# Kernel optimization log

Hardware: AMD Instinct MI355X
Metric: run time of the kernel (lower is better)

Reference implementation:

```python
import jax, jax.numpy as jnp
import numpy as np

B, S, D = 2, 2048, 512
H = 8
HD = D // H  # head dim = 64


def setup_inputs() -> dict:
    key = jax.random.key(0)
    ks = jax.random.split(key, 4)
    scale = 1.0 / np.sqrt(D)
    x = jax.random.normal(ks[0], (B, S, D), dtype=jnp.float32)
    wq = jax.random.normal(ks[1], (D, D), dtype=jnp.float32) * scale
    wk = jax.random.normal(ks[2], (D, D), dtype=jnp.float32) * scale
    wv = jax.random.normal(ks[3], (D, D), dtype=jnp.float32) * scale
    bq = jnp.zeros((D,), dtype=jnp.float32)
    bk = jnp.zeros((D,), dtype=jnp.float32)
    bv = jnp.zeros((D,), dtype=jnp.float32)
    return {"x": x, "wq": wq, "bq": bq, "wk": wk, "bk": bk, "wv": wv, "bv": bv}


def reference(x, wq, bq, wk, bk, wv, bv):
    # Linear projections (torch Linear: y = x @ W^T + b; weights here stored as [out,in])
    q = x @ wq.T + bq  # [B,S,D]
    k = x @ wk.T + bk
    v = x @ wv.T + bv
    # split heads -> [B,H,S,HD]
    q = q.reshape(B, S, H, HD).transpose(0, 2, 1, 3)
    k = k.reshape(B, S, H, HD).transpose(0, 2, 1, 3)
    v = v.reshape(B, S, H, HD).transpose(0, 2, 1, 3)
    # QK^T scores, scaled by 1/sqrt(head_dim)
    scores = jnp.einsum("bhqd,bhkd->bhqk", q, k) / jnp.sqrt(jnp.float32(HD))
    # softmax-free: elementwise sigmoid instead of softmax normalization
    attn = jax.nn.sigmoid(scores)  # [B,H,S,S] — the memory-bound intermediate
    out = jnp.einsum("bhqk,bhkd->bhqd", attn, v)
    # merge heads -> [B,S,D]
    return out.transpose(0, 2, 1, 3).reshape(B, S, D)
```

## Files before the change

kernel.cpp:

```cpp
#include <hip/hip_runtime.h>
#include <cstdint>
#include <cstddef>

#define BB   2
#define SS   2048
#define DD   512
#define HH   8
#define HDIM 64
#define XN   ((size_t)BB * SS * DD)
#define WN   ((size_t)DD * DD)

typedef __attribute__((ext_vector_type(8)))  short          s16x8;
typedef __attribute__((ext_vector_type(8)))  unsigned short u16x8;
typedef __attribute__((ext_vector_type(16))) float          f32x16;

static __device__ __forceinline__ unsigned short f2bf(float f) {
  union { float f; unsigned u; } x; x.f = f;
  unsigned r = x.u + 0x7fffu + ((x.u >> 16) & 1u);
  return (unsigned short)(r >> 16);
}
static __device__ __forceinline__ unsigned packtrunc(float lo, float hi) {
  return __builtin_amdgcn_perm(__float_as_uint(hi), __float_as_uint(lo), 0x07060302u);
}

#define QSCALE (-0.18033688011111543f)

__global__ __launch_bounds__(256) void cvt_kernel(
    const float* __restrict__ x,
    const float* __restrict__ wq, const float* __restrict__ wk, const float* __restrict__ wv,
    unsigned short* __restrict__ xb, unsigned short* __restrict__ wb3) {
  const int y = blockIdx.y;
  const float* src; unsigned short* dst;
  if (y == 0) { src = x; dst = xb; }
  else {
    if (blockIdx.x >= 256) return;
    src = (y == 1) ? wq : (y == 2) ? wk : wv;
    dst = wb3 + (size_t)(y - 1) * WN;
  }
  int i = (blockIdx.x * 256 + threadIdx.x) * 4;
  float4 f = *(const float4*)(src + i);
  ushort4 o;
  o.x = f2bf(f.x); o.y = f2bf(f.y); o.z = f2bf(f.z); o.w = f2bf(f.w);
  *(ushort4*)(dst + i) = o;
}

__global__ __launch_bounds__(256) void proj_kernel(
    const unsigned short* __restrict__ xb, const unsigned short* __restrict__ wb3,
    const float* __restrict__ bq, const float* __restrict__ bk, const float* __restrict__ bv,
    unsigned short* __restrict__ qo, unsigned short* __restrict__ ko,
    unsigned short* __restrict__ vt) {
  __shared__ unsigned short As[2][128 * 40];
  __shared__ unsigned short Bs[2][64 * 40];

  const int z = blockIdx.z;
  const unsigned short* w = wb3 + (size_t)z * WN;
  const float* bias = (z == 0) ? bq : (z == 1) ? bk : bv;

  const int t = threadIdx.x;
  const int lane = t & 63, wave = t >> 6;
  const int ln = lane & 31, hi = lane >> 5;
  const int m0 = blockIdx.x * 128, n0 = blockIdx.y * 64;

  u16x8 ar[2], br;
#pragma unroll
  for (int i = 0; i < 2; i++) {
    int c = t + i * 256;
    ar[i] = *(const u16x8*)&xb[(size_t)(m0 + (c >> 2)) * DD + (c & 3) * 8];
  }
  br = *(const u16x8*)&w[(size_t)(n0 + (t >> 2)) * DD + (t & 3) * 8];
#pragma unroll
  for (int i = 0; i < 2; i++) {
    int c = t + i * 256;
    *(u16x8*)&As[0][(c >> 2) * 40 + (c & 3) * 8] = ar[i];
  }
  *(u16x8*)&Bs[0][(t >> 2) * 40 + (t & 3) * 8] = br;
  __syncthreads();

  f32x16 acc0 = {}, acc1 = {};

#pragma unroll 2
  for (int kt = 0; kt < 16; kt++) {
    const int cur = kt & 1, nxt = cur ^ 1;
    if (kt < 15) {
      int k0 = (kt + 1) * 32;
#pragma unroll
      for (int i = 0; i < 2; i++) {
        int c = t + i * 256;
        ar[i] = *(const u16x8*)&xb[(size_t)(m0 + (c >> 2)) * DD + k0 + (c & 3) * 8];
      }
      br = *(const u16x8*)&w[(size_t)(n0 + (t >> 2)) * DD + k0 + (t & 3) * 8];
    }
#pragma unroll
    for (int cc = 0; cc < 2; cc++) {
      s16x8 af = *(const s16x8*)&As[cur][(wave * 32 + ln) * 40 + cc * 16 + hi * 8];
      s16x8 b0 = *(const s16x8*)&Bs[cur][(ln) * 40 + cc * 16 + hi * 8];
      s16x8 b1 = *(const s16x8*)&Bs[cur][(32 + ln) * 40 + cc * 16 + hi * 8];
      acc0 = __builtin_amdgcn_mfma_f32_32x32x16_bf16(af, b0, acc0, 0, 0, 0);
      acc1 = __builtin_amdgcn_mfma_f32_32x32x16_bf16(af, b1, acc1, 0, 0, 0);
    }
    if (kt < 15) {
#pragma unroll
      for (int i = 0; i < 2; i++) {
        int c = t + i * 256;
        *(u16x8*)&As[nxt][(c >> 2) * 40 + (c & 3) * 8] = ar[i];
      }
      *(u16x8*)&Bs[nxt][(t >> 2) * 40 + (t & 3) * 8] = br;
    }
    __syncthreads();
  }

  const int h = blockIdx.y;
  const int bidx = m0 >> 11;
  const int sbase = (m0 & 2047) + wave * 32;
  const size_t bhb = (size_t)(bidx * HH + h) * SS * HDIM;
  const int kts = sbase >> 5;

#pragma unroll
  for (int nh = 0; nh < 2; nh++) {
    f32x16 acc = nh ? acc1 : acc0;
    const int hd = nh * 32 + ln;
    const float bval = bias[n0 + hd];

    if (z == 0) {
#pragma unroll
      for (int r = 0; r < 16; r++) {
        int s = sbase + (r & 3) + 8 * (r >> 2) + 4 * hi;
        qo[bhb + (size_t)s * HDIM + hd] = f2bf((acc[r] + bval) * QSCALE);
      }
    } else if (z == 1) {
      const int c = hd >> 4, hk = (hd >> 3) & 1, j = hd & 7;
      unsigned short* kd = ko + bhb + ((size_t)kts * 4 + c) * 512 + j;
#pragma unroll
      for (int r = 0; r < 16; r++) {
        int off = (r & 3) + 8 * (r >> 2) + 4 * hi;
        kd[(hk * 32 + off) * 8] = f2bf(acc[r] + bval);
      }
    } else {
      unsigned short* vd = vt + bhb + ((size_t)kts * 4 + nh * 2) * 512 + hi * 256 + ln * 8;
#pragma unroll
      for (int g = 0; g < 4; g++) {
        unsigned short* vg = vd + (g >> 1) * 512 + (g & 1) * 4;
#pragma unroll
        for (int j = 0; j < 4; j += 2) {
          unsigned pk = (unsigned)f2bf(acc[g * 4 + j] + bval) |
                        ((unsigned)f2bf(acc[g * 4 + j + 1] + bval) << 16);
          *(unsigned*)&vg[j] = pk;
        }
      }
    }
  }
}

__global__ __launch_bounds__(512, 4) void attn_kernel(
    const unsigned short* __restrict__ qb,
    const unsigned short* __restrict__ kfb,
    const unsigned short* __restrict__ vfb,
    float* __restrict__ out) {
  __shared__ __align__(16) float red[2 * 4096];

  const int t = threadIdx.x;
  const int lane = t & 63, wave = t >> 6;
  const int ln = lane & 31, hi = lane >> 5;
  const int qh = wave & 1, kh = wave >> 1;
  const int fid = blockIdx.y * 32 + blockIdx.x;
  const int bh = fid & 15, qx = fid >> 4;
  const int b = bh >> 3, h = bh & 7;
  const unsigned short* qp = qb + (size_t)bh * SS * HDIM;
  const unsigned short* kfp = kfb + (size_t)bh * SS * HDIM;
  const unsigned short* vfp = vfb + (size_t)bh * SS * HDIM;
  const int q0 = qx * 64;

  s16x8 qf[4];
#pragma unroll
  for (int c = 0; c < 4; c++)
    qf[c] = *(const s16x8*)&qp[(size_t)(q0 + qh * 32 + ln) * HDIM + c * 16 + hi * 8];

  f32x16 o0 = {}, o1 = {};

  s16x8 kf[4], vf[4];
  int foff = kh * 16 * 2048 + lane * 8;
#pragma unroll
  for (int c = 0; c < 4; c++) {
    kf[c] = *(const s16x8*)&kfp[foff + c * 512];
    vf[c] = *(const s16x8*)&vfp[foff + c * 512];
  }
  foff += 2048;

#pragma unroll 1
  for (int i = 0; i < 16; i++) {
    f32x16 st = {};
#pragma unroll
    for (int c = 0; c < 4; c++)
      st = __builtin_amdgcn_mfma_f32_32x32x16_bf16(kf[c], qf[c], st, 0, 0, 0);

    if (i < 15) {
#pragma unroll
      for (int c = 0; c < 4; c++)
        kf[c] = *(const s16x8*)&kfp[foff + c * 512];
    }

    unsigned pg[8];
#pragma unroll
    for (int g = 0; g < 4; g++) {
      float p0 = __builtin_amdgcn_rcpf(1.0f + __builtin_amdgcn_exp2f(st[4 * g + 0]));
      float p1 = __builtin_amdgcn_rcpf(1.0f + __builtin_amdgcn_exp2f(st[4 * g + 1]));
      float p2 = __builtin_amdgcn_rcpf(1.0f + __builtin_amdgcn_exp2f(st[4 * g + 2]));
      float p3 = __builtin_amdgcn_rcpf(1.0f + __builtin_amdgcn_exp2f(st[4 * g + 3]));
      pg[2 * g]     = packtrunc(p0, p1);
      pg[2 * g + 1] = packtrunc(p2, p3);
    }

#pragma unroll
    for (int c = 0; c < 2; c++) {
      union { unsigned u[4]; s16x8 v; } pu;
      pu.u[0] = pg[4 * c + 0];
      pu.u[1] = pg[4 * c + 1];
      pu.u[2] = pg[4 * c + 2];
      pu.u[3] = pg[4 * c + 3];
      o0 = __builtin_amdgcn_mfma_f32_32x32x16_bf16(pu.v, vf[c], o0, 0, 0, 0);
      o1 = __builtin_amdgcn_mfma_f32_32x32x16_bf16(pu.v, vf[2 + c], o1, 0, 0, 0);
    }

    if (i < 15) {
#pragma unroll
      for (int c = 0; c < 4; c++)
        vf[c] = *(const s16x8*)&vfp[foff + c * 512];
      foff += 2048;
    }
  }

  if (kh >= 2) {
    const int slot = kh - 2;
#pragma unroll
    for (int dh = 0; dh < 2; dh++) {
      f32x16 ov = dh ? o1 : o0;
#pragma unroll
      for (int r = 0; r < 16; r++) {
        int ql = (r & 3) + 8 * (r >> 2) + 4 * hi;
        red[slot * 4096 + (qh * 32 + ql) * 64 + dh * 32 + ln] = ov[r];
      }
    }
  }
  __syncthreads();
  if (kh < 2) {
#pragma unroll
    for (int dh = 0; dh < 2; dh++) {
      f32x16 ov = dh ? o1 : o0;
#pragma unroll
      for (int r = 0; r < 16; r++) {
        int ql = (r & 3) + 8 * (r >> 2) + 4 * hi;
        red[kh * 4096 + (qh * 32 + ql) * 64 + dh * 32 + ln] += ov[r];
      }
    }
  }
  __syncthreads();
  const float4* r0 = (const float4*)red;
  const float4* r1 = (const float4*)(red + 4096);
#pragma unroll
  for (int j = 0; j < 2; j++) {
    int g = t + j * 512;
    float4 s0 = r0[g], s1 = r1[g];
    float4 s;
    s.x = s0.x + s1.x; s.y = s0.y + s1.y; s.z = s0.z + s1.z; s.w = s0.w + s1.w;
    int q = g >> 4, dbase = (g & 15) * 4;
    *(float4*)&out[((size_t)(b * SS + q0 + q)) * DD + h * HDIM + dbase] = s;
  }
}

extern "C" void kernel_launch(void* const* d_in, const int* in_sizes, int n_in,
                              void* d_out, int out_size, void* d_ws, size_t ws_size,
                              hipStream_t stream) {
  const float* x  = (const float*)d_in[0];
  const float* wq = (const float*)d_in[1];
  const float* bq = (const float*)d_in[2];
  const float* wk = (const float*)d_in[3];
  const float* bk = (const float*)d_in[4];
  const float* wv = (const float*)d_in[5];
  const float* bv = (const float*)d_in[6];
  float* out = (float*)d_out;

  unsigned short* xb = (unsigned short*)d_ws;
  unsigned short* wb = xb + XN;
  unsigned short* qo = wb + 3 * WN;
  unsigned short* ko = qo + XN;
  unsigned short* vt = ko + XN;

  cvt_kernel<<<dim3(2048, 4), 256, 0, stream>>>(x, wq, wk, wv, xb, wb);
  proj_kernel<<<dim3(32, 8, 3), 256, 0, stream>>>(xb, wb, bq, bk, bv, qo, ko, vt);
  attn_kernel<<<dim3(SS / 64, BB * HH), 512, 0, stream>>>(qo, ko, vt, out);
}
```

Measured before the change: 113.5 us.

## Process two query sub-tiles per wave to reuse K/V fragments in attention

```diff
diff --git a/kernel.cpp b/kernel.cpp
--- a/kernel.cpp
+++ b/kernel.cpp
@@ -151,31 +151,33 @@
   }
 }
 
-__global__ __launch_bounds__(512, 4) void attn_kernel(
+__global__ __launch_bounds__(512, 2) void attn_kernel(
     const unsigned short* __restrict__ qb,
     const unsigned short* __restrict__ kfb,
     const unsigned short* __restrict__ vfb,
     float* __restrict__ out) {
-  __shared__ __align__(16) float red[2 * 4096];
+  __shared__ __align__(16) float red[2 * 8192];
 
   const int t = threadIdx.x;
   const int lane = t & 63, wave = t >> 6;
   const int ln = lane & 31, hi = lane >> 5;
-  const int qh = wave & 1, kh = wave >> 1;
-  const int fid = blockIdx.y * 32 + blockIdx.x;
+  const int qp = wave & 1, kh = wave >> 1;
+  const int fid = blockIdx.y * 16 + blockIdx.x;
   const int bh = fid & 15, qx = fid >> 4;
   const int b = bh >> 3, h = bh & 7;
-  const unsigned short* qp = qb + (size_t)bh * SS * HDIM;
+  const unsigned short* qp_ = qb + (size_t)bh * SS * HDIM;
   const unsigned short* kfp = kfb + (size_t)bh * SS * HDIM;
   const unsigned short* vfp = vfb + (size_t)bh * SS * HDIM;
-  const int q0 = qx * 64;
-
-  s16x8 qf[4];
-#pragma unroll
-  for (int c = 0; c < 4; c++)
-    qf[c] = *(const s16x8*)&qp[(size_t)(q0 + qh * 32 + ln) * HDIM + c * 16 + hi * 8];
-
-  f32x16 o0 = {}, o1 = {};
+  const int q0 = qx * 128 + qp * 64;
+
+  s16x8 qf[2][4];
+#pragma unroll
+  for (int qs = 0; qs < 2; qs++)
+#pragma unroll
+    for (int c = 0; c < 4; c++)
+      qf[qs][c] = *(const s16x8*)&qp_[(size_t)(q0 + qs * 32 + ln) * HDIM + c * 16 + hi * 8];
+
+  f32x16 o00 = {}, o01 = {}, o10 = {}, o11 = {};
 
   s16x8 kf[4], vf[4];
   int foff = kh * 16 * 2048 + lane * 8;
@@ -188,10 +190,12 @@
 
 #pragma unroll 1
   for (int i = 0; i < 16; i++) {
-    f32x16 st = {};
-#pragma unroll
-    for (int c = 0; c < 4; c++)
-      st = __builtin_amdgcn_mfma_f32_32x32x16_bf16(kf[c], qf[c], st, 0, 0, 0);
+    f32x16 st0 = {}, st1 = {};
+#pragma unroll
+    for (int c = 0; c < 4; c++) {
+      st0 = __builtin_amdgcn_mfma_f32_32x32x16_bf16(kf[c], qf[0][c], st0, 0, 0, 0);
+      st1 = __builtin_amdgcn_mfma_f32_32x32x16_bf16(kf[c], qf[1][c], st1, 0, 0, 0);
+    }
 
     if (i < 15) {
 #pragma unroll
@@ -199,26 +203,38 @@
         kf[c] = *(const s16x8*)&kfp[foff + c * 512];
     }
 
-    unsigned pg[8];
-#pragma unroll
-    for (int g = 0; g < 4; g++) {
-      float p0 = __builtin_amdgcn_rcpf(1.0f + __builtin_amdgcn_exp2f(st[4 * g + 0]));
-      float p1 = __builtin_amdgcn_rcpf(1.0f + __builtin_amdgcn_exp2f(st[4 * g + 1]));
-      float p2 = __builtin_amdgcn_rcpf(1.0f + __builtin_amdgcn_exp2f(st[4 * g + 2]));
-      float p3 = __builtin_amdgcn_rcpf(1.0f + __builtin_amdgcn_exp2f(st[4 * g + 3]));
-      pg[2 * g]     = packtrunc(p0, p1);
-      pg[2 * g + 1] = packtrunc(p2, p3);
+    unsigned pg[2][8];
+#pragma unroll
+    for (int qs = 0; qs < 2; qs++) {
+      f32x16 st = qs ? st1 : st0;
+#pragma unroll
+      for (int g = 0; g < 4; g++) {
+        float p0 = __builtin_amdgcn_rcpf(1.0f + __builtin_amdgcn_exp2f(st[4 * g + 0]));
+        float p1 = __builtin_amdgcn_rcpf(1.0f + __builtin_amdgcn_exp2f(st[4 * g + 1]));
+        float p2 = __builtin_amdgcn_rcpf(1.0f + __builtin_amdgcn_exp2f(st[4 * g + 2]));
+        float p3 = __builtin_amdgcn_rcpf(1.0f + __builtin_amdgcn_exp2f(st[4 * g + 3]));
+        pg[qs][2 * g]     = packtrunc(p0, p1);
+        pg[qs][2 * g + 1] = packtrunc(p2, p3);
+      }
     }
 
 #pragma unroll
     for (int c = 0; c < 2; c++) {
-      union { unsigned u[4]; s16x8 v; } pu;
-      pu.u[0] = pg[4 * c + 0];
-      pu.u[1] = pg[4 * c + 1];
-      pu.u[2] = pg[4 * c + 2];
-      pu.u[3] = pg[4 * c + 3];
-      o0 = __builtin_amdgcn_mfma_f32_32x32x16_bf16(pu.v, vf[c], o0, 0, 0, 0);
-      o1 = __builtin_amdgcn_mfma_f32_32x32x16_bf16(pu.v, vf[2 + c], o1, 0, 0, 0);
+#pragma unroll
+      for (int qs = 0; qs < 2; qs++) {
+        union { unsigned u[4]; s16x8 v; } pu;
+        pu.u[0] = pg[qs][4 * c + 0];
+        pu.u[1] = pg[qs][4 * c + 1];
+        pu.u[2] = pg[qs][4 * c + 2];
+        pu.u[3] = pg[qs][4 * c + 3];
+        if (qs == 0) {
+          o00 = __builtin_amdgcn_mfma_f32_32x32x16_bf16(pu.v, vf[c], o00, 0, 0, 0);
+          o01 = __builtin_amdgcn_mfma_f32_32x32x16_bf16(pu.v, vf[2 + c], o01, 0, 0, 0);
+        } else {
+          o10 = __builtin_amdgcn_mfma_f32_32x32x16_bf16(pu.v, vf[c], o10, 0, 0, 0);
+          o11 = __builtin_amdgcn_mfma_f32_32x32x16_bf16(pu.v, vf[2 + c], o11, 0, 0, 0);
+        }
+      }
     }
 
     if (i < 15) {
@@ -230,40 +246,46 @@
   }
 
   if (kh >= 2) {
-    const int slot = kh - 2;
-#pragma unroll
-    for (int dh = 0; dh < 2; dh++) {
-      f32x16 ov = dh ? o1 : o0;
-#pragma unroll
-      for (int r = 0; r < 16; r++) {
-        int ql = (r & 3) + 8 * (r >> 2) + 4 * hi;
-        red[slot * 4096 + (qh * 32 + ql) * 64 + dh * 32 + ln] = ov[r];
-      }
-    }
+    float* slot = red + (kh - 2) * 8192;
+#pragma unroll
+    for (int qs = 0; qs < 2; qs++)
+#pragma unroll
+      for (int dh = 0; dh < 2; dh++) {
+        f32x16 ov = qs ? (dh ? o11 : o10) : (dh ? o01 : o00);
+#pragma unroll
+        for (int r = 0; r < 16; r++) {
+          int ql = qp * 64 + qs * 32 + (r & 3) + 8 * (r >> 2) + 4 * hi;
+          slot[ql * 64 + dh * 32 + ln] = ov[r];
+        }
+      }
   }
   __syncthreads();
   if (kh < 2) {
-#pragma unroll
-    for (int dh = 0; dh < 2; dh++) {
-      f32x16 ov = dh ? o1 : o0;
-#pragma unroll
-      for (int r = 0; r < 16; r++) {
-        int ql = (r & 3) + 8 * (r >> 2) + 4 * hi;
-        red[kh * 4096 + (qh * 32 + ql) * 64 + dh * 32 + ln] += ov[r];
-      }
-    }
+    float* slot = red + kh * 8192;
+#pragma unroll
+    for (int qs = 0; qs < 2; qs++)
+#pragma unroll
+      for (int dh = 0; dh < 2; dh++) {
+        f32x16 ov = qs ? (dh ? o11 : o10) : (dh ? o01 : o00);
+#pragma unroll
+        for (int r = 0; r < 16; r++) {
+          int ql = qp * 64 + qs * 32 + (r & 3) + 8 * (r >> 2) + 4 * hi;
+          slot[ql * 64 + dh * 32 + ln] += ov[r];
+        }
+      }
   }
   __syncthreads();
   const float4* r0 = (const float4*)red;
-  const float4* r1 = (const float4*)(red + 4096);
-#pragma unroll
-  for (int j = 0; j < 2; j++) {
+  const float4* r1 = (const float4*)(red + 8192);
+  const int qblk = qx * 128;
+#pragma unroll
+  for (int j = 0; j < 4; j++) {
     int g = t + j * 512;
     float4 s0 = r0[g], s1 = r1[g];
     float4 s;
     s.x = s0.x + s1.x; s.y = s0.y + s1.y; s.z = s0.z + s1.z; s.w = s0.w + s1.w;
     int q = g >> 4, dbase = (g & 15) * 4;
-    *(float4*)&out[((size_t)(b * SS + q0 + q)) * DD + h * HDIM + dbase] = s;
+    *(float4*)&out[((size_t)(b * SS + qblk + q)) * DD + h * HDIM + dbase] = s;
   }
 }
 
@@ -287,5 +309,5 @@
 
   cvt_kernel<<<dim3(2048, 4), 256, 0, stream>>>(x, wq, wk, wv, xb, wb);
   proj_kernel<<<dim3(32, 8, 3), 256, 0, stream>>>(xb, wb, bq, bk, bv, qo, ko, vt);
-  attn_kernel<<<dim3(SS / 64, BB * HH), 512, 0, stream>>>(qo, ko, vt, out);
-}
+  attn_kernel<<<dim3(SS / 128, BB * HH), 512, 0, stream>>>(qo, ko, vt, out);
+}
```

After: 112.6 us. About the same (-0.8%).
